# Performance work log

Hardware: AMD Instinct MI355X
Metric: run time of the kernel (lower is better)

Reference implementation:

```python
import jax, jax.numpy as jnp
import numpy as np

NUM_LAYERS = 4   # i: conv layers in Unary
K_DISP = 128     # k: disparity labels
FEAT_C = 64      # unary feature channels


def _conv3x3(x, w, b):
    # x: [B,C,H,W], w: [O,I,3,3] (OIHW), padding SAME, stride 1
    y = jax.lax.conv_general_dilated(
        x, w, window_strides=(1, 1), padding='SAME',
        dimension_numbers=('NCHW', 'OIHW', 'NCHW'))
    return y + b[None, :, None, None]


def _unary(x, Ws, bs):
    # i conv layers, tanh between layers, linear output (siamese unary net)
    n = len(Ws)
    for i in range(n):
        x = _conv3x3(x, Ws[i], bs[i])
        if i < n - 1:
            x = jnp.tanh(x)
    return x


def _correlation(phiL, phiR, k):
    # corr[b,d,y,x] = sum_c phiL[b,c,y,x] * phiR[b,c,y,x-d], zero out-of-range
    B, C, H, W = phiL.shape
    Rpad = jnp.pad(phiR, ((0, 0), (0, 0), (0, 0), (k - 1, 0)))  # zero-pad left

    def step(_, d):
        # shifted right feature map: Rpad[..., k-1-d : k-1-d+W] == phiR shifted right by d
        Rs = jax.lax.dynamic_slice_in_dim(Rpad, k - 1 - d, W, axis=3)
        return None, jnp.einsum('bchw,bchw->bhw', phiL, Rs)

    _, ys = jax.lax.scan(step, None, jnp.arange(k))  # [k,B,H,W]
    return jnp.moveaxis(ys, 0, 1)                    # [B,k,H,W]


def setup_inputs() -> dict:
    key = jax.random.key(0)
    ks = jax.random.split(key, 2 + NUM_LAYERS)
    B, H, W = 2, 384, 1280
    d = {
        'l': jax.random.normal(ks[0], (B, 3, H, W), jnp.float32),
        'r': jax.random.normal(ks[1], (B, 3, H, W), jnp.float32),
    }
    chans = [3] + [FEAT_C] * NUM_LAYERS

    def xavier(k_, shape):
        fan_in = shape[1] * shape[2] * shape[3]
        fan_out = shape[0] * shape[2] * shape[3]
        std = float(np.sqrt(2.0 / (fan_in + fan_out)))
        return jax.random.normal(k_, shape, jnp.float32) * std

    for i in range(NUM_LAYERS):
        d[f'W{i}'] = xavier(ks[2 + i], (chans[i + 1], chans[i], 3, 3))
        d[f'b{i}'] = jnp.zeros((chans[i + 1],), jnp.float32)
    return d


def reference(l, r, W0, b0, W1, b1, W2, b2, W3, b3):
    Ws = [W0, W1, W2, W3]
    bs = [b0, b1, b2, b3]
    phi_left = _unary(l, Ws, bs)
    phi_right = _unary(r, Ws, bs)
    return _correlation(phi_left, phi_right, K_DISP)  # [B, k, H, W]
```

## Files before the change

### kernel.cpp

```cpp
#include <hip/hip_runtime.h>

#define HH 384
#define WW 1280

typedef unsigned short u16;
typedef unsigned int u32;
typedef __attribute__((ext_vector_type(8))) short short8;
typedef __attribute__((ext_vector_type(8))) unsigned short u16x8;
typedef __attribute__((ext_vector_type(4))) float f32x4;

__device__ __forceinline__ float bf2f(u16 u){ union{u32 i;float f;}v; v.i=((u32)u)<<16; return v.f; }
__device__ __forceinline__ u16 f2bf(float f){ union{float f;u32 i;}v; v.f=f; u32 r=v.i+0x7fffu+((v.i>>16)&1u); return (u16)(r>>16); }
__device__ __forceinline__ float ftanh(float x){
  float e = __expf(2.0f*x);
  return 1.0f - 2.0f/(e+1.0f);
}
__device__ __forceinline__ void gload_lds16(const void* g, void* l){
  __builtin_amdgcn_global_load_lds((const __attribute__((address_space(1))) void*)g,
                                   (__attribute__((address_space(3))) void*)l, 16, 0, 0);
}

__global__ __launch_bounds__(256) void prep_weights(const float* __restrict__ W1,
    const float* __restrict__ W2, const float* __restrict__ W3,
    const float* __restrict__ W0, u16* __restrict__ wf, u16* __restrict__ wq0){
  int idx = blockIdx.x*256 + threadIdx.x;
  if (idx < 110592){
    int m    = idx & 63;
    int oc   = (idx>>6) & 63;
    int tap  = (idx>>12) % 9;
    int layer= idx / 36864;
    int ic   = m ^ ((oc&7)<<3);
    const float* Ws = layer==0 ? W1 : (layer==1 ? W2 : W3);
    wf[idx] = f2bf(Ws[(oc*64+ic)*9 + tap]);
  } else if (idx < 110592 + 2048){
    int j  = idx - 110592;
    int k  = j & 31;
    int oc = j >> 5;
    u16 v = 0;
    if (k < 27){
      int ic = k/9, rem = k - ic*9, dy = rem/3, dx = rem - dy*3;
      v = f2bf(W0[(oc*3+ic)*9 + dy*3 + dx]);
    }
    wq0[j] = v;
  }
}

__global__ __launch_bounds__(256) void conv0_kernel(const float* __restrict__ l,
    const float* __restrict__ r, const u16* __restrict__ wq0,
    const float* __restrict__ b0, u16* __restrict__ out){
  const int tid = threadIdx.x;
  const int x0 = blockIdx.x*64;
  const int y0 = blockIdx.y*4;
  const int n  = blockIdx.z;
  const float* img = (n < 2 ? l : r) + (size_t)(n & 1)*3*HH*WW;

  const int lane = tid & 63;
  const int wv  = tid >> 6;
  const int l15 = lane & 15;
  const int lh  = lane >> 4;
  const int y   = y0 + wv;

  const float* rowp[8];
  int dxm1[8];
  #pragma unroll
  for (int e=0; e<8; ++e){
    int k  = lh*8 + e;
    int ic = k/9, rem = k - ic*9, dy = rem/3, dx = rem - dy*3;
    int gy = y + dy - 1;
    bool ok = (k < 27) && ((unsigned)gy < (unsigned)HH);
    rowp[e] = ok ? (img + ((size_t)ic*HH + gy)*WW) : (const float*)0;
    dxm1[e] = dx - 1;
  }

  short8 b[4];
  #pragma unroll
  for (int nt=0; nt<4; ++nt)
    b[nt] = *(const short8*)(wq0 + (size_t)(nt*16 + l15)*32 + lh*8);

  short8 a[4];
  #pragma unroll
  for (int mt=0; mt<4; ++mt){
    int xb = x0 + mt*16 + l15;
    float v[8];
    #pragma unroll
    for (int e=0; e<8; ++e){
      int gx = xb + dxm1[e];
      const float* p = rowp[e];
      bool ok = (p != 0) && ((unsigned)gx < (unsigned)WW);
      v[e] = ok ? p[gx] : 0.f;
    }
    short8 af;
    #pragma unroll
    for (int e=0; e<8; ++e) af[e] = (short)f2bf(v[e]);
    a[mt] = af;
  }

  f32x4 acc[4][4];
  #pragma unroll
  for (int mt=0;mt<4;++mt)
    #pragma unroll
    for (int nt=0;nt<4;++nt) acc[mt][nt] = (f32x4){0.f,0.f,0.f,0.f};
  #pragma unroll
  for (int mt=0; mt<4; ++mt)
    #pragma unroll
    for (int nt=0; nt<4; ++nt)
      acc[mt][nt] = __builtin_amdgcn_mfma_f32_16x16x32_bf16(a[mt], b[nt], acc[mt][nt], 0,0,0);

  float bv[4];
  #pragma unroll
  for (int nt=0;nt<4;++nt) bv[nt] = b0[nt*16 + l15];
  u16* outR = out + (size_t)n*HH*WW*64 + (size_t)y*WW*64;
  #pragma unroll
  for (int mt=0; mt<4; ++mt){
    #pragma unroll
    for (int rr=0; rr<4; ++rr){
      int x = x0 + mt*16 + lh*4 + rr;
      u16* op = outR + (size_t)x*64 + l15;
      #pragma unroll
      for (int nt=0; nt<4; ++nt){
        float v = acc[mt][nt][rr] + bv[nt];
        v = ftanh(v);
        op[nt*16] = f2bf(v);
      }
    }
  }
}

template<bool TANH>
__global__ __launch_bounds__(256) void conv64_kernel(const u16* __restrict__ in,
    const u16* __restrict__ wfL, const float* __restrict__ bias,
    const u16* __restrict__ zpad, u16* __restrict__ out){
  __shared__ __align__(16) u16 tile[6*66*64];
  __shared__ __align__(16) u16 wbuf[3][4096];
  const int tid = threadIdx.x;
  int id = blockIdx.x;
  id = (id & 7)*960 + (id >> 3);
  const int x0 = (id % 20)*64;
  const int y0 = ((id / 20) % 96)*4;
  const int n  = id / 1920;
  const u16* inN = in + (size_t)n*HH*WW*64;

  for (int q0 = 0; q0 < 3168; q0 += 256){
    int q = q0 + tid;
    if (q < 3168){
      int row = q / 528;
      int rem = q - row*528;
      int col = rem >> 3;
      int j   = rem & 7;
      int gy = y0 - 1 + row;
      int gx = x0 - 1 + col;
      const u16* g;
      if ((unsigned)gy < (unsigned)HH && (unsigned)gx < (unsigned)WW)
        g = inN + (((size_t)(gy*WW + gx))<<6) + ((j ^ (col&7))<<3);
      else
        g = zpad + (j<<3);
      gload_lds16(g, &tile[(size_t)(q & ~63)*8]);
    }
  }
  #pragma unroll
  for (int t=0; t<2; ++t)
    #pragma unroll
    for (int c=0; c<2; ++c){
      int q = c*256 + tid;
      gload_lds16(wfL + (size_t)t*4096 + (size_t)q*8, &wbuf[t][(q & ~63)*8]);
    }
  asm volatile("s_waitcnt vmcnt(2)" ::: "memory");
  __builtin_amdgcn_s_barrier();
  __builtin_amdgcn_sched_barrier(0);

  const int lane = tid & 63;
  const int wv = tid >> 6;
  const int l15 = lane & 15;
  const int lh  = lane >> 4;

  f32x4 acc[4][4];
  #pragma unroll
  for (int mt=0;mt<4;++mt)
    #pragma unroll
    for (int nt=0;nt<4;++nt) acc[mt][nt] = (f32x4){0.f,0.f,0.f,0.f};

  #pragma unroll
  for (int tap = 0; tap < 9; ++tap){
    const int dy = tap/3, dx = tap%3;
    if (tap <= 6){
      const u16* wsrc = wfL + (size_t)(tap+2)*4096;
      u16* wdst = wbuf[(tap+2)%3];
      #pragma unroll
      for (int c=0;c<2;++c){
        int q = c*256 + tid;
        gload_lds16(wsrc + (size_t)q*8, &wdst[(q & ~63)*8]);
      }
    }
    const char* wb = (const char*)wbuf[tap%3];
    const char* tb = (const char*)tile;
    const int xorA = ((l15 + dx)&7)<<4;
    const int xorB = (l15&7)<<4;
    #pragma unroll
    for (int kh=0; kh<2; ++kh){
      const int kbyte = kh*64 + lh*16;
      short8 a[4], b[4];
      #pragma unroll
      for (int mt=0; mt<4; ++mt){
        int col = mt*16 + l15 + dx;
        a[mt] = *(const short8*)(tb + ((wv+dy)*66 + col)*128 + (kbyte ^ xorA));
      }
      #pragma unroll
      for (int nt=0; nt<4; ++nt){
        int oc = nt*16 + l15;
        b[nt] = *(const short8*)(wb + oc*128 + (kbyte ^ xorB));
      }
      #pragma unroll
      for (int mt=0; mt<4; ++mt)
        #pragma unroll
        for (int nt=0; nt<4; ++nt)
          acc[mt][nt] = __builtin_amdgcn_mfma_f32_16x16x32_bf16(a[mt], b[nt], acc[mt][nt], 0,0,0);
    }
    if (tap < 8){
      if (tap <= 6) asm volatile("s_waitcnt vmcnt(2)" ::: "memory");
      else          asm volatile("s_waitcnt vmcnt(0)" ::: "memory");
      __builtin_amdgcn_s_barrier();
      __builtin_amdgcn_sched_barrier(0);
    }
  }

  float bv[4];
  #pragma unroll
  for (int nt=0;nt<4;++nt) bv[nt] = bias[nt*16 + l15];
  const int gy = y0 + wv;
  u16* outR = out + (size_t)n*HH*WW*64 + (size_t)gy*WW*64;
  #pragma unroll
  for (int mt=0; mt<4; ++mt){
    #pragma unroll
    for (int r=0; r<4; ++r){
      int x = x0 + mt*16 + lh*4 + r;
      u16* op = outR + (size_t)x*64 + l15;
      #pragma unroll
      for (int nt=0; nt<4; ++nt){
        float v = acc[mt][nt][r] + bv[nt];
        if (TANH) v = ftanh(v);
        op[nt*16] = f2bf(v);
      }
    }
  }
}

__global__ __launch_bounds__(256) void corr_kernel(const u16* __restrict__ phi,
    float* __restrict__ out){
  __shared__ __align__(16) float band[128*65];
  const int tid = threadIdx.x;
  int id = blockIdx.x;
  id = (id & 7)*1920 + (id >> 3);
  const int x0 = (id % 20)*64;
  const int y  = (id / 20) % 384;
  const int b  = id / 7680;
  const u16* Lrow = phi + ((size_t)((b    )*HH + y)*WW)*64;
  const u16* Rrow = phi + ((size_t)((b + 2)*HH + y)*WW)*64;

  const int lane = tid & 63;
  const int wv   = tid >> 6;
  const int l15  = lane & 15;
  const int lh   = lane >> 4;

  f32x4 acc[4][3];
  #pragma unroll
  for (int mt=0;mt<4;++mt)
    #pragma unroll
    for (int nt=0;nt<3;++nt) acc[mt][nt] = (f32x4){0.f,0.f,0.f,0.f};

  #pragma unroll
  for (int kh=0; kh<2; ++kh){
    const int koff = kh*32 + lh*8;
    short8 a[4], bb[3];
    #pragma unroll
    for (int mt=0; mt<4; ++mt)
      a[mt] = *(const short8*)(Lrow + (size_t)(x0 + mt*16 + l15)*64 + koff);
    #pragma unroll
    for (int nt=0; nt<3; ++nt){
      int gx = x0 - 128 + wv*48 + nt*16 + l15;
      short8 z = (short8){0,0,0,0,0,0,0,0};
      bb[nt] = (gx >= 0) ? *(const short8*)(Rrow + (size_t)gx*64 + koff) : z;
    }
    #pragma unroll
    for (int mt=0; mt<4; ++mt)
      #pragma unroll
      for (int nt=0; nt<3; ++nt)
        acc[mt][nt] = __builtin_amdgcn_mfma_f32_16x16x32_bf16(a[mt], bb[nt], acc[mt][nt], 0,0,0);
  }

  #pragma unroll
  for (int mt=0; mt<4; ++mt){
    #pragma unroll
    for (int nt=0; nt<3; ++nt){
      int jr = wv*48 + nt*16 + l15;
      #pragma unroll
      for (int r=0; r<4; ++r){
        int x = mt*16 + lh*4 + r;
        int d = x - jr + 128;
        if ((unsigned)d < 128u) band[d*65 + x] = acc[mt][nt][r];
      }
    }
  }
  __syncthreads();

  float* ob = out + ((size_t)(b*128)*HH + (size_t)y)*WW + x0;
  #pragma unroll
  for (int it=0; it<8; ++it){
    int c = it*256 + tid;
    int d = c>>4, xq = c&15;
    const float* bp = &band[d*65 + xq*4];
    float4 v = make_float4(bp[0], bp[1], bp[2], bp[3]);
    *(float4*)&ob[(size_t)d*HH*WW + xq*4] = v;
  }
}

extern "C" void kernel_launch(void* const* d_in, const int* in_sizes, int n_in,
                              void* d_out, int out_size, void* d_ws, size_t ws_size,
                              hipStream_t stream){
  const float* l  = (const float*)d_in[0];
  const float* r  = (const float*)d_in[1];
  const float* W0 = (const float*)d_in[2];
  const float* b0 = (const float*)d_in[3];
  const float* W1 = (const float*)d_in[4];
  const float* b1 = (const float*)d_in[5];
  const float* W2 = (const float*)d_in[6];
  const float* b2 = (const float*)d_in[7];
  const float* W3 = (const float*)d_in[8];
  const float* b3 = (const float*)d_in[9];
  float* out = (float*)d_out;

  u16* wf   = (u16*)d_ws;
  u16* wq0  = (u16*)((char*)d_ws + (512u<<10));
  u16* zpad = (u16*)((char*)d_ws + (1u<<20));
  u16* B    = (u16*)((char*)d_ws + (2u<<20));
  u16* A    = (u16*)d_out;

  hipMemsetAsync(zpad, 0, 256, stream);
  prep_weights<<<dim3(440), dim3(256), 0, stream>>>(W1, W2, W3, W0, wf, wq0);

  conv0_kernel<<<dim3(20, 96, 4), dim3(256), 0, stream>>>(l, r, wq0, b0, A);
  conv64_kernel<true ><<<dim3(7680), dim3(256), 0, stream>>>(A, wf + 0*36864, b1, zpad, B);
  conv64_kernel<true ><<<dim3(7680), dim3(256), 0, stream>>>(B, wf + 1*36864, b2, zpad, A);
  conv64_kernel<false><<<dim3(7680), dim3(256), 0, stream>>>(A, wf + 2*36864, b3, zpad, B);

  corr_kernel<<<dim3(15360), dim3(256), 0, stream>>>(B, out);
}
```

Before: 853.6 us.

## Fuse first two conv layers, keeping layer-0 output with halo in LDS

Measured after the change: 882.0 us. 3.3% more time.

```diff
diff --git a/kernel.cpp b/kernel.cpp
--- a/kernel.cpp
+++ b/kernel.cpp
@@ -45,71 +45,159 @@
   }
 }
 
-__global__ __launch_bounds__(256) void conv0_kernel(const float* __restrict__ l,
+__global__ __launch_bounds__(256) void conv01_kernel(const float* __restrict__ l,
     const float* __restrict__ r, const u16* __restrict__ wq0,
-    const float* __restrict__ b0, u16* __restrict__ out){
+    const float* __restrict__ b0, const u16* __restrict__ wfL,
+    const float* __restrict__ bias, u16* __restrict__ out){
+  __shared__ __align__(16) u16 tile[6*66*64];
+  __shared__ __align__(16) u16 wbuf[3][4096];
+  float* FB = (float*)&wbuf[2][0];
   const int tid = threadIdx.x;
-  const int x0 = blockIdx.x*64;
-  const int y0 = blockIdx.y*4;
-  const int n  = blockIdx.z;
+  int id = blockIdx.x;
+  id = (id & 7)*960 + (id >> 3);
+  const int x0 = (id % 20)*64;
+  const int y0 = ((id / 20) % 96)*4;
+  const int n  = id / 1920;
   const float* img = (n < 2 ? l : r) + (size_t)(n & 1)*3*HH*WW;
 
   const int lane = tid & 63;
   const int wv  = tid >> 6;
   const int l15 = lane & 15;
   const int lh  = lane >> 4;
-  const int y   = y0 + wv;
-
-  const float* rowp[8];
-  int dxm1[8];
-  #pragma unroll
-  for (int e=0; e<8; ++e){
-    int k  = lh*8 + e;
-    int ic = k/9, rem = k - ic*9, dy = rem/3, dx = rem - dy*3;
-    int gy = y + dy - 1;
-    bool ok = (k < 27) && ((unsigned)gy < (unsigned)HH);
-    rowp[e] = ok ? (img + ((size_t)ic*HH + gy)*WW) : (const float*)0;
-    dxm1[e] = dx - 1;
-  }
-
-  short8 b[4];
-  #pragma unroll
-  for (int nt=0; nt<4; ++nt)
-    b[nt] = *(const short8*)(wq0 + (size_t)(nt*16 + l15)*32 + lh*8);
-
-  short8 a[4];
-  #pragma unroll
-  for (int mt=0; mt<4; ++mt){
-    int xb = x0 + mt*16 + l15;
-    float v[8];
-    #pragma unroll
-    for (int e=0; e<8; ++e){
-      int gx = xb + dxm1[e];
-      const float* p = rowp[e];
-      bool ok = (p != 0) && ((unsigned)gx < (unsigned)WW);
-      v[e] = ok ? p[gx] : 0.f;
-    }
-    short8 af;
-    #pragma unroll
-    for (int e=0; e<8; ++e) af[e] = (short)f2bf(v[e]);
-    a[mt] = af;
-  }
+
+  short8 wf0[4];
+  #pragma unroll
+  for (int mo=0; mo<4; ++mo)
+    wf0[mo] = *(const short8*)(wq0 + (size_t)(mo*16 + l15)*32 + lh*8);
+  float4 bv0[4];
+  #pragma unroll
+  for (int mo=0; mo<4; ++mo) bv0[mo] = *(const float4*)&b0[mo*16 + lh*4];
+
+  #pragma unroll
+  for (int it=0; it<7; ++it){
+    int e = it*256 + tid;
+    if (e < 1632){
+      int ch  = e / 544;
+      int rem = e - ch*544;
+      int row = rem / 68;
+      int col = rem - row*68;
+      int gy = y0 - 2 + row, gx = x0 - 2 + col;
+      float v = 0.f;
+      if ((unsigned)gy < (unsigned)HH && (unsigned)gx < (unsigned)WW)
+        v = img[((size_t)ch*HH + gy)*WW + gx];
+      FB[e] = v;
+    }
+  }
+#define PREFW(t) do{ \
+    _Pragma("unroll") \
+    for (int c=0;c<2;++c){ \
+      int q = c*256 + tid; \
+      gload_lds16(wfL + (size_t)(t)*4096 + (size_t)q*8, &wbuf[(t)%3][(q & ~63)*8]); \
+    } }while(0)
+  PREFW(0); PREFW(1);
+  __syncthreads();
+
+  int icE[8], dyE[8], dxE[8]; bool okE[8];
+  #pragma unroll
+  for (int e=0;e<8;++e){
+    int k = lh*8+e;
+    okE[e] = (k < 27);
+    int kk = okE[e] ? k : 0;
+    icE[e] = kk/9; int rem = kk - icE[e]*9; dyE[e] = rem/3; dxE[e] = rem - dyE[e]*3;
+  }
+
+  #pragma unroll
+  for (int i=0; i<8; ++i){
+    int U = i*4 + wv;
+    if (U < 30){
+      int ry = U/5, cf = U - ry*5;
+      int p  = cf*16 + l15 - 1;
+      float v[8];
+      #pragma unroll
+      for (int e=0;e<8;++e){
+        int fcol = cf*16 + l15 + dxE[e]; if (fcol > 67) fcol = 67;
+        int frow = ry + dyE[e];
+        float t = FB[icE[e]*544 + frow*68 + fcol];
+        v[e] = okE[e] ? t : 0.f;
+      }
+      short8 xf;
+      #pragma unroll
+      for (int e=0;e<8;++e) xf[e] = (short)f2bf(v[e]);
+      f32x4 acc0[4];
+      #pragma unroll
+      for (int mo=0;mo<4;++mo){
+        acc0[mo] = (f32x4){0.f,0.f,0.f,0.f};
+        acc0[mo] = __builtin_amdgcn_mfma_f32_16x16x32_bf16(wf0[mo], xf, acc0[mo], 0,0,0);
+      }
+      if (p <= 64){
+        int tcol = p + 1;
+        int orow = y0 - 1 + ry;
+        int gxo  = x0 + p;
+        bool okpx = ((unsigned)orow < (unsigned)HH) && ((unsigned)gxo < (unsigned)WW);
+        char* tb = (char*)tile;
+        #pragma unroll
+        for (int mo=0;mo<4;++mo){
+          float t0 = okpx ? ftanh(acc0[mo][0] + bv0[mo].x) : 0.f;
+          float t1 = okpx ? ftanh(acc0[mo][1] + bv0[mo].y) : 0.f;
+          float t2 = okpx ? ftanh(acc0[mo][2] + bv0[mo].z) : 0.f;
+          float t3 = okpx ? ftanh(acc0[mo][3] + bv0[mo].w) : 0.f;
+          ushort4 pv;
+          pv.x = f2bf(t0); pv.y = f2bf(t1); pv.z = f2bf(t2); pv.w = f2bf(t3);
+          *(ushort4*)(tb + (ry*66 + tcol)*128 + ((mo*32 + lh*8) ^ ((tcol&7)<<4))) = pv;
+        }
+      }
+    }
+  }
+  __syncthreads();
 
   f32x4 acc[4][4];
   #pragma unroll
   for (int mt=0;mt<4;++mt)
     #pragma unroll
     for (int nt=0;nt<4;++nt) acc[mt][nt] = (f32x4){0.f,0.f,0.f,0.f};
-  #pragma unroll
-  for (int mt=0; mt<4; ++mt)
-    #pragma unroll
-    for (int nt=0; nt<4; ++nt)
-      acc[mt][nt] = __builtin_amdgcn_mfma_f32_16x16x32_bf16(a[mt], b[nt], acc[mt][nt], 0,0,0);
+
+  #pragma unroll
+  for (int tap = 0; tap < 9; ++tap){
+    const int dy = tap/3, dx = tap%3;
+    if (tap <= 6){ PREFW(tap+2); }
+    const char* wb = (const char*)wbuf[tap%3];
+    const char* tb = (const char*)tile;
+    const int xorA = ((l15 + dx)&7)<<4;
+    const int xorB = (l15&7)<<4;
+    #pragma unroll
+    for (int kh=0; kh<2; ++kh){
+      const int kbyte = kh*64 + lh*16;
+      short8 a[4], b[4];
+      #pragma unroll
+      for (int mt=0; mt<4; ++mt){
+        int col = mt*16 + l15 + dx;
+        a[mt] = *(const short8*)(tb + ((wv+dy)*66 + col)*128 + (kbyte ^ xorA));
+      }
+      #pragma unroll
+      for (int nt=0; nt<4; ++nt){
+        int oc = nt*16 + l15;
+        b[nt] = *(const short8*)(wb + oc*128 + (kbyte ^ xorB));
+      }
+      #pragma unroll
+      for (int mt=0; mt<4; ++mt)
+        #pragma unroll
+        for (int nt=0; nt<4; ++nt)
+          acc[mt][nt] = __builtin_amdgcn_mfma_f32_16x16x32_bf16(a[mt], b[nt], acc[mt][nt], 0,0,0);
+    }
+    if (tap < 8){
+      if (tap <= 6) asm volatile("s_waitcnt vmcnt(2)" ::: "memory");
+      else          asm volatile("s_waitcnt vmcnt(0)" ::: "memory");
+      __builtin_amdgcn_s_barrier();
+      __builtin_amdgcn_sched_barrier(0);
+    }
+  }
+#undef PREFW
 
   float bv[4];
   #pragma unroll
-  for (int nt=0;nt<4;++nt) bv[nt] = b0[nt*16 + l15];
-  u16* outR = out + (size_t)n*HH*WW*64 + (size_t)y*WW*64;
+  for (int nt=0;nt<4;++nt) bv[nt] = bias[nt*16 + l15];
+  const int gy = y0 + wv;
+  u16* outR = out + (size_t)n*HH*WW*64 + (size_t)gy*WW*64;
   #pragma unroll
   for (int mt=0; mt<4; ++mt){
     #pragma unroll
@@ -337,8 +425,7 @@
   hipMemsetAsync(zpad, 0, 256, stream);
   prep_weights<<<dim3(440), dim3(256), 0, stream>>>(W1, W2, W3, W0, wf, wq0);
 
-  conv0_kernel<<<dim3(20, 96, 4), dim3(256), 0, stream>>>(l, r, wq0, b0, A);
-  conv64_kernel<true ><<<dim3(7680), dim3(256), 0, stream>>>(A, wf + 0*36864, b1, zpad, B);
+  conv01_kernel<<<dim3(7680), dim3(256), 0, stream>>>(l, r, wq0, b0, wf + 0*36864, b1, B);
   conv64_kernel<true ><<<dim3(7680), dim3(256), 0, stream>>>(B, wf + 1*36864, b2, zpad, A);
   conv64_kernel<false><<<dim3(7680), dim3(256), 0, stream>>>(A, wf + 2*36864, b3, zpad, B);
 
```
